# Kernel optimization log

Hardware: AMD Instinct MI355X
Metric: run time of the kernel (lower is better)

Reference implementation:

```python
import jax, jax.numpy as jnp
import numpy as np

B_, S_, D_ = 2, 1024, 1024
EXPAND = 2
D_INNER = EXPAND * D_            # 2048
HEADDIM = 64
NHEADS = D_INNER // HEADDIM      # 32
D_STATE = 64
NGROUPS = 1
D_CONV = 4
CONV_DIM = D_INNER + 2 * NGROUPS * D_STATE      # 2176
D_IN_PROJ = 2 * D_INNER + 2 * NGROUPS * D_STATE + NHEADS  # 4256
H_MLP = 8 * D_                   # GatedMLP fc_1 out (scale * d_model)


def setup_inputs() -> dict:
    key = jax.random.key(0)
    ks = jax.random.split(key, 12)
    n = lambda k, shp, s=0.02: jax.random.normal(k, shp, dtype=jnp.float32) * s
    return {
        "x": jax.random.normal(ks[0], (B_, S_, D_), dtype=jnp.float32),
        "in_proj_w": n(ks[1], (D_IN_PROJ, D_)),
        "conv_w": n(ks[2], (CONV_DIM, D_CONV), 0.2),
        "conv_b": jnp.zeros((CONV_DIM,), jnp.float32),
        "dt_bias": jax.random.normal(ks[3], (NHEADS,), dtype=jnp.float32) * 0.5 - 2.0,
        "A_log": jnp.log(1.0 + 15.0 * jax.random.uniform(ks[4], (NHEADS,), dtype=jnp.float32)),
        "D": jax.random.normal(ks[5], (NHEADS,), dtype=jnp.float32) * 0.1 + 1.0,
        "ssm_norm_w": jnp.ones((D_INNER,), jnp.float32),
        "out_proj_w": n(ks[6], (D_, D_INNER)),
        "rms_w": jnp.ones((D_,), jnp.float32),
        "fc1_w": n(ks[7], (H_MLP, D_)),
        "fc2_w": n(ks[8], (D_, H_MLP // 2)),
    }


def _rms(x, w, eps=1e-5):
    return x * jax.lax.rsqrt(jnp.mean(x * x, axis=-1, keepdims=True) + eps) * w


def _mamba(x, in_proj_w, conv_w, conv_b, dt_bias, A_log, D, ssm_norm_w, out_proj_w):
    b, s, _ = x.shape
    zxbcdt = x @ in_proj_w.T                         # [b,s,D_IN_PROJ]
    z = zxbcdt[..., :D_INNER]
    xBC = zxbcdt[..., D_INNER:D_INNER + CONV_DIM]
    dt_raw = zxbcdt[..., -NHEADS:]
    # causal depthwise conv1d + SiLU
    xc = jnp.pad(jnp.transpose(xBC, (0, 2, 1)), ((0, 0), (0, 0), (D_CONV - 1, 0)))
    xc = jax.lax.conv_general_dilated(xc, conv_w[:, None, :], (1,), 'VALID',
                                      feature_group_count=CONV_DIM,
                                      dimension_numbers=('NCH', 'OIH', 'NCH'))
    xBC = jax.nn.silu(jnp.transpose(xc, (0, 2, 1)) + conv_b)
    xs = xBC[..., :D_INNER].reshape(b, s, NHEADS, HEADDIM)
    Bm = xBC[..., D_INNER:D_INNER + D_STATE]         # [b,s,n] (ngroups=1)
    Cm = xBC[..., D_INNER + D_STATE:]
    dt = jax.nn.softplus(dt_raw + dt_bias)           # [b,s,h]
    dA = jnp.exp(dt * (-jnp.exp(A_log)))             # [b,s,h]
    dtx = dt[..., None] * xs                          # [b,s,h,p]

    def step(h, inp):
        dA_t, dtx_t, B_t, C_t = inp
        h = h * dA_t[:, :, None, None] + jnp.einsum('bhp,bn->bhpn', dtx_t, B_t)
        y = jnp.einsum('bhpn,bn->bhp', h, C_t)
        return h, y

    h0 = jnp.zeros((b, NHEADS, HEADDIM, D_STATE), x.dtype)
    _, y = jax.lax.scan(step, h0, (jnp.transpose(dA, (1, 0, 2)),
                                   jnp.transpose(dtx, (1, 0, 2, 3)),
                                   jnp.transpose(Bm, (1, 0, 2)),
                                   jnp.transpose(Cm, (1, 0, 2))))
    y = jnp.transpose(y, (1, 0, 2, 3)) + D[None, None, :, None] * xs
    y = y.reshape(b, s, D_INNER) * jax.nn.silu(z)    # gated
    y = _rms(y, ssm_norm_w)
    return y @ out_proj_w.T


def reference(x, in_proj_w, conv_w, conv_b, dt_bias, A_log, D, ssm_norm_w,
              out_proj_w, rms_w, fc1_w, fc2_w):
    # x = x + mamba(x)
    x = x + _mamba(x, in_proj_w, conv_w, conv_b, dt_bias, A_log, D, ssm_norm_w, out_proj_w)
    # x = x + GatedMLP(RMSNorm(x))
    xn = _rms(x, rms_w)
    h1 = xn @ fc1_w.T
    a, g = jnp.split(h1, 2, axis=-1)
    m = (a * jax.nn.silu(g)) @ fc2_w.T
    return x + m
```

## Files before the change

kernel.cpp:

```cpp
#include <hip/hip_runtime.h>
#include <math.h>

typedef unsigned short u16;
typedef __attribute__((ext_vector_type(8))) __bf16 bf16x8;
typedef __attribute__((ext_vector_type(4))) float f32x4;
typedef __attribute__((ext_vector_type(4))) u16 u16x4;
typedef __attribute__((ext_vector_type(8))) u16 u16x8;
typedef __attribute__((ext_vector_type(4))) float float4v;

constexpr int kS = 1024;
constexpr int kD = 1024;
constexpr int kDinner = 2048;
constexpr int kHeads = 32;
constexpr int kConvDim = 2176;
constexpr int kDproj = 4256;
constexpr int kDprojPad = 4352;
constexpr int kRows = 2048;
constexpr int kHmlp = 8192;
constexpr int kHhalf = 4096;
constexpr int kL = 64;
constexpr int kNC = 16;

__device__ __forceinline__ float bf2f(u16 u) {
    return __builtin_bit_cast(float, (unsigned int)u << 16);
}
__device__ __forceinline__ u16 f2bf(float f) {
    unsigned int u = __builtin_bit_cast(unsigned int, f);
    u += 0x7fffu + ((u >> 16) & 1u);
    return (u16)(u >> 16);
}
__device__ __forceinline__ float silu_(float x) { return x / (1.f + __expf(-x)); }

__device__ __forceinline__ void gld16(const u16* g, u16* l) {
    __builtin_amdgcn_global_load_lds(
        (const __attribute__((address_space(1))) void*)g,
        (__attribute__((address_space(3))) void*)l, 16, 0, 0);
}

constexpr int kB1 = kRows * kD / 4;
constexpr int kB2 = kB1 + kDprojPad * kD / 4;
constexpr int kB3 = kB2 + kD * kDinner / 4;
constexpr int kB4 = kB3 + kHmlp * kD / 4;
constexpr int kB5 = kB4 + kD * kHhalf / 4;
__global__ __launch_bounds__(256)
void cast_all_kernel(const float* __restrict__ x, const float* __restrict__ w1,
                     const float* __restrict__ w2, const float* __restrict__ w3,
                     const float* __restrict__ w4, u16* __restrict__ xbf,
                     u16* __restrict__ w1bf, u16* __restrict__ w2bf,
                     u16* __restrict__ w3bf, u16* __restrict__ w4bf) {
    int i = blockIdx.x * 256 + threadIdx.x;
    const float* src;
    u16* dst;
    int j;
    if (i < kB1) {
        j = i; src = x; dst = xbf;
    } else if (i < kB2) {
        j = i - kB1;
        int e = j * 4, row = e >> 10, col = e & 1023;
        u16x4 o = {0, 0, 0, 0};
        if (row < kDproj) {
            float4v v = *(const float4v*)(w1 + (size_t)row * kD + col);
            o.x = f2bf(v.x); o.y = f2bf(v.y); o.z = f2bf(v.z); o.w = f2bf(v.w);
        }
        ((u16x4*)w1bf)[j] = o;
        return;
    } else if (i < kB3) {
        j = i - kB2; src = w2; dst = w2bf;
    } else if (i < kB4) {
        j = i - kB3;
        int e = j * 4, row = e >> 10, col4 = (e & 1023) >> 2;
        int p = (row < kHhalf) ? row : row - kHhalf;
        int permrow = (p >> 4) * 32 + (p & 15) + ((row < kHhalf) ? 0 : 16);
        float4v v = ((const float4v*)w3)[j];
        u16x4 o;
        o.x = f2bf(v.x); o.y = f2bf(v.y); o.z = f2bf(v.z); o.w = f2bf(v.w);
        ((u16x4*)w3bf)[permrow * 256 + col4] = o;
        return;
    } else {
        j = i - kB4; src = w4; dst = w4bf;
    }
    float4v v = ((const float4v*)src)[j];
    u16x4 o;
    o.x = f2bf(v.x); o.y = f2bf(v.y); o.z = f2bf(v.z); o.w = f2bf(v.w);
    ((u16x4*)dst)[j] = o;
}

template <bool OUT_BF16, bool GATED = false>
__global__ __launch_bounds__(256)
void gemm_bt(const u16* __restrict__ A, const u16* __restrict__ W,
             void* __restrict__ Cout, const float* __restrict__ resid,
             int M, int N, int K) {
    __shared__ u16 As[2][128 * 32];
    __shared__ u16 Bs[2][128 * 32];
    const int tid = threadIdx.x;
    const int lane = tid & 63;
    const int w = __builtin_amdgcn_readfirstlane(tid >> 6);
    const int wm = w >> 1, wn = w & 1;
    const int bm = blockIdx.y * 128;
    const int bn = blockIdx.x * 128;
    const int z = blockIdx.z;
    const int Kchunk = K / gridDim.z;
    const int k0 = z * Kchunk;

    f32x4 acc[4][4];
#pragma unroll
    for (int i = 0; i < 4; i++)
#pragma unroll
        for (int j = 0; j < 4; j++) acc[i][j] = {0.f, 0.f, 0.f, 0.f};

    const int srow = lane >> 2;
    const int scol = (lane & 3) * 8;
    const u16* gA = A + (size_t)(bm + w * 32 + srow) * K + k0 + scol;
    const u16* gB = W + (size_t)(bn + w * 32 + srow) * K + k0 + scol;
    const size_t rstep = (size_t)16 * K;

    const int sbase0 = (w * 32) * 32;
    const int sbase1 = (w * 32 + 16) * 32;
    const int fra = (lane & 15) * 32 + (lane >> 4) * 8;

    gld16(gA, &As[0][sbase0]);
    gld16(gA + rstep, &As[0][sbase1]);
    gld16(gB, &Bs[0][sbase0]);
    gld16(gB + rstep, &Bs[0][sbase1]);

    const int nk = Kchunk >> 5;
    for (int i = 0; i < nk; i++) {
        const int cur = i & 1, nxt = cur ^ 1;
        __syncthreads();
        if (i + 1 < nk) {
            int kt2 = (i + 1) * 32;
            gld16(gA + kt2, &As[nxt][sbase0]);
            gld16(gA + kt2 + rstep, &As[nxt][sbase1]);
            gld16(gB + kt2, &Bs[nxt][sbase0]);
            gld16(gB + kt2 + rstep, &Bs[nxt][sbase1]);
        }
        bf16x8 av[4], bv[4];
#pragma unroll
        for (int mi = 0; mi < 4; mi++)
            av[mi] = *(const bf16x8*)&As[cur][(wm * 64 + mi * 16) * 32 + fra];
#pragma unroll
        for (int ni = 0; ni < 4; ni++)
            bv[ni] = *(const bf16x8*)&Bs[cur][(wn * 64 + ni * 16) * 32 + fra];
#pragma unroll
        for (int mi = 0; mi < 4; mi++)
#pragma unroll
            for (int ni = 0; ni < 4; ni++)
                acc[mi][ni] = __builtin_amdgcn_mfma_f32_16x16x32_bf16(av[mi], bv[ni], acc[mi][ni], 0, 0, 0);
    }

    const int rb = bm + wm * 64 + ((lane >> 4) << 2);
    const int cb = bn + wn * 64 + (lane & 15);
    if (GATED) {
        u16* Cb = (u16*)Cout;
        const int NG = N >> 1;
        const int gc0 = ((bn + wn * 64) >> 1) + (lane & 15);
#pragma unroll
        for (int mi = 0; mi < 4; mi++) {
#pragma unroll
            for (int p = 0; p < 2; p++) {
#pragma unroll
                for (int r = 0; r < 4; r++) {
                    float a = acc[mi][2 * p][r];
                    float g = acc[mi][2 * p + 1][r];
                    Cb[(size_t)(rb + mi * 16 + r) * NG + gc0 + p * 16] =
                        f2bf(a * silu_(g));
                }
            }
        }
        return;
    }
    float* Cf = (float*)Cout + (size_t)z * M * N;
    u16* Cb = (u16*)Cout;
#pragma unroll
    for (int mi = 0; mi < 4; mi++) {
#pragma unroll
        for (int ni = 0; ni < 4; ni++) {
#pragma unroll
            for (int r = 0; r < 4; r++) {
                size_t offo = (size_t)(rb + mi * 16 + r) * N + (cb + ni * 16);
                float v = acc[mi][ni][r];
                if (resid) v += resid[offo];
                if (OUT_BF16) Cb[offo] = f2bf(v);
                else Cf[offo] = v;
            }
        }
    }
}

__global__ __launch_bounds__(256)
void splitk_reduce_kernel(const float* __restrict__ Cp, const float* __restrict__ resid,
                          float* __restrict__ out, int mn4) {
    int i = blockIdx.x * 256 + threadIdx.x;
    if (i >= mn4) return;
    constexpr size_t MN = (size_t)kRows * kD;
    float4v s0 = ((const float4v*)Cp)[i];
    float4v s1 = ((const float4v*)(Cp + MN))[i];
    float4v s2 = ((const float4v*)(Cp + 2 * MN))[i];
    float4v s3 = ((const float4v*)(Cp + 3 * MN))[i];
    float4v r = ((const float4v*)resid)[i];
    float4v o;
    o.x = s0.x + s1.x + s2.x + s3.x + r.x;
    o.y = s0.y + s1.y + s2.y + s3.y + r.y;
    o.z = s0.z + s1.z + s2.z + s3.z + r.z;
    o.w = s0.w + s1.w + s2.w + s3.w + r.w;
    ((float4v*)out)[i] = o;
}

__global__ __launch_bounds__(256)
void reduce_rms_kernel(const float* __restrict__ Cp, const float* __restrict__ resid,
                       float* __restrict__ x2, const float* __restrict__ rmsw,
                       u16* __restrict__ xnbf) {
    const int row = blockIdx.x;
    const int tid = threadIdx.x;
    constexpr size_t MN = (size_t)kRows * kD;
    size_t i = (size_t)row * (kD / 4) + tid;
    float4v s0 = ((const float4v*)Cp)[i];
    float4v s1 = ((const float4v*)(Cp + MN))[i];
    float4v s2 = ((const float4v*)(Cp + 2 * MN))[i];
    float4v s3 = ((const float4v*)(Cp + 3 * MN))[i];
    float4v r = ((const float4v*)resid)[i];
    float4v v;
    v.x = s0.x + s1.x + s2.x + s3.x + r.x;
    v.y = s0.y + s1.y + s2.y + s3.y + r.y;
    v.z = s0.z + s1.z + s2.z + s3.z + r.z;
    v.w = s0.w + s1.w + s2.w + s3.w + r.w;
    ((float4v*)x2)[i] = v;
    float ss = v.x * v.x + v.y * v.y + v.z * v.z + v.w * v.w;
#pragma unroll
    for (int off = 32; off > 0; off >>= 1) ss += __shfl_down(ss, off);
    __shared__ float red[4];
    int wv = tid >> 6, lane = tid & 63;
    if (lane == 0) red[wv] = ss;
    __syncthreads();
    ss = red[0] + red[1] + red[2] + red[3];
    float rstd = rsqrtf(ss * (1.f / kD) + 1e-5f);
    float4v wv4 = ((const float4v*)rmsw)[tid];
    u16x4 o;
    o.x = f2bf(v.x * rstd * wv4.x);
    o.y = f2bf(v.y * rstd * wv4.y);
    o.z = f2bf(v.z * rstd * wv4.z);
    o.w = f2bf(v.w * rstd * wv4.w);
    ((u16x4*)xnbf)[i] = o;
}

__global__ __launch_bounds__(256)
void convdt_kernel(const u16* __restrict__ zxbf, const float* __restrict__ convw,
                   const float* __restrict__ convb, u16* __restrict__ xsbf,
                   float* __restrict__ BCf, const float* __restrict__ dt_bias,
                   const float* __restrict__ A_log, float* __restrict__ dtf,
                   float* __restrict__ dAf) {
    int c = blockIdx.x * 256 + threadIdx.x;
    int row = blockIdx.y;
    if (c >= kConvDim + kHeads) return;
    if (c < kConvDim) {
        int s = row & (kS - 1);
        float acc = convb[c];
#pragma unroll
        for (int j = 0; j < 4; j++) {
            int sj = s - 3 + j;
            if (sj >= 0)
                acc += bf2f(zxbf[(size_t)(row - 3 + j) * kDprojPad + kDinner + c]) * convw[c * 4 + j];
        }
        float v = silu_(acc);
        if (c < kDinner) xsbf[(size_t)row * kDinner + c] = f2bf(v);
        else BCf[(size_t)row * 128 + (c - kDinner)] = v;
    } else {
        int h = c - kConvDim;
        float raw = bf2f(zxbf[(size_t)row * kDprojPad + (kDinner + kConvDim) + h]) + dt_bias[h];
        float dt = (raw > 20.f) ? raw : log1pf(__expf(raw));
        float dA = __expf(-dt * __expf(A_log[h]));
        dtf[(size_t)row * kHeads + h] = dt;
        dAf[(size_t)row * kHeads + h] = dA;
    }
}

__global__ __launch_bounds__(256)
void scan_chunk_kernel(const u16* __restrict__ xsbf, const float* __restrict__ BCf,
                       const float* __restrict__ dtf, const float* __restrict__ dAf,
                       const float* __restrict__ Dv, u16* __restrict__ ysbf,
                       float* __restrict__ Pf, float* __restrict__ Scf) {
    const int c = blockIdx.x, h = blockIdx.y, b = blockIdx.z;
    const int tid = threadIdx.x;
    const int lane = tid & 63;
    const int nq = tid >> 6;
    const int p = nq * 16 + (lane & 15);
    const int ng = lane >> 4;

    __shared__ float BC_lds[kL * 136];
    __shared__ u16 xs_lds[kL * 64];
    __shared__ float dA_lds[kL];
    __shared__ float dt_lds[kL];
    __shared__ u16 ybuf[kL * 64];

    const int row0 = b * kS + c * kL;

#pragma unroll
    for (int i = 0; i < 8; i++) {
        int e4 = i * 256 + tid;
        int t = e4 >> 5;
        int col = (e4 & 31) * 4;
        float4v v = *(const float4v*)(BCf + (size_t)(row0 + t) * 128 + col);
        int dst = t * 136 + (col < 64 ? col : col + 4);
        *(float4v*)&BC_lds[dst] = v;
    }
#pragma unroll
    for (int i = 0; i < 2; i++) {
        int e8 = i * 256 + tid;
        int t = e8 >> 3, col8 = (e8 & 7) * 8;
        *(u16x8*)&xs_lds[t * 64 + col8] =
            *(const u16x8*)(xsbf + (size_t)(row0 + t) * kDinner + h * 64 + col8);
    }
    if (tid < kL) {
        dt_lds[tid] = dtf[(size_t)(row0 + tid) * kHeads + h];
        dA_lds[tid] = dAf[(size_t)(row0 + tid) * kHeads + h];
    }
    __syncthreads();

    float hst[16];
#pragma unroll
    for (int j = 0; j < 16; j++) hst[j] = 0.f;
    float P = 1.f;
    const float Dh = Dv[h];

    for (int t = 0; t < kL; t++) {
        float dAv = dA_lds[t];
        float dtv = dt_lds[t];
        float xsv = bf2f(xs_lds[t * 64 + p]);
        float dtx = dtv * xsv;
        P *= dAv;
        const float* Bt = &BC_lds[t * 136 + ng * 16];
        const float* Ct = Bt + 68;
        float yp = 0.f;
#pragma unroll
        for (int j = 0; j < 16; j++) {
            float Bn = Bt[j];
            float Cn = Ct[j];
            hst[j] = hst[j] * dAv + dtx * Bn;
            yp += hst[j] * Cn;
        }
        yp += __shfl_xor(yp, 16);
        yp += __shfl_xor(yp, 32);
        if (ng == 0) ybuf[t * 64 + p] = f2bf(yp + Dh * xsv);
        if (tid == 0) Pf[(size_t)(row0 + t) * kHeads + h] = P;
    }
    __syncthreads();

#pragma unroll
    for (int i = 0; i < 2; i++) {
        int e8 = i * 256 + tid;
        int t = e8 >> 3, col8 = (e8 & 7) * 8;
        *(u16x8*)(ysbf + (size_t)(row0 + t) * kDinner + h * 64 + col8) =
            *(u16x8*)&ybuf[t * 64 + col8];
    }
    const int bhc = (b * 32 + h) * kNC + c;
    float* Sdst = Scf + (size_t)bhc * 4096 + p * 64 + ng * 16;
#pragma unroll
    for (int j = 0; j < 16; j += 4) {
        f32x4 v = {hst[j], hst[j + 1], hst[j + 2], hst[j + 3]};
        *(f32x4*)(Sdst + j) = v;
    }
}

__global__ __launch_bounds__(256)
void chunk_state_kernel(const float* __restrict__ Scf, const float* __restrict__ Pf,
                        float* __restrict__ Hinf) {
    const int bh = blockIdx.x;
    const int b = bh >> 5, h = bh & 31;
    const int tid = threadIdx.x;
    float hreg[16];
#pragma unroll
    for (int k = 0; k < 16; k++) hreg[k] = 0.f;
    for (int c = 0; c < kNC - 1; c++) {
        float Q = Pf[(size_t)(b * kS + c * kL + kL - 1) * kHeads + h];
        size_t sbase = (size_t)(bh * kNC + c) * 4096;
        size_t dbase = (size_t)(bh * kNC + c + 1) * 4096;
#pragma unroll
        for (int k = 0; k < 16; k++) {
            float s = Scf[sbase + k * 256 + tid];
            hreg[k] = Q * hreg[k] + s;
            Hinf[dbase + k * 256 + tid] = hreg[k];
        }
    }
}

__global__ __launch_bounds__(256)
void chunk_corr_kernel(const float* __restrict__ Hinf, const float* __restrict__ BCf,
                       const float* __restrict__ Pf, u16* __restrict__ ysbf) {
    const int c = blockIdx.x + 1;
    const int h = blockIdx.y, b = blockIdx.z;
    const int tid = threadIdx.x;
    const int lane = tid & 63, wq = tid >> 6;
    __shared__ float Hin_lds[64 * 65];
    __shared__ float C_lds[kL * 64];
    const int bh = b * 32 + h;
    const size_t hbase = (size_t)(bh * kNC + c) * 4096;
#pragma unroll
    for (int k = 0; k < 16; k++) {
        int e = k * 256 + tid;
        Hin_lds[(e >> 6) * 65 + (e & 63)] = Hinf[hbase + e];
    }
    const int row0 = b * kS + c * kL;
#pragma unroll
    for (int k = 0; k < 4; k++) {
        int e4 = k * 256 + tid;
        int t = e4 >> 4, n4 = (e4 & 15) * 4;
        *(float4v*)&C_lds[t * 64 + n4] =
            *(const float4v*)(BCf + (size_t)(row0 + t) * 128 + 64 + n4);
    }
    __syncthreads();

    float hr[64];
#pragma unroll
    for (int n = 0; n < 64; n++) hr[n] = Hin_lds[lane * 65 + n];

    for (int tt = 0; tt < 16; tt++) {
        int t = wq * 16 + tt;
        float corr = 0.f;
#pragma unroll
        for (int n4 = 0; n4 < 16; n4++) {
            float4v cv = *(const float4v*)&C_lds[t * 64 + n4 * 4];
            corr += cv.x * hr[n4 * 4] + cv.y * hr[n4 * 4 + 1] +
                    cv.z * hr[n4 * 4 + 2] + cv.w * hr[n4 * 4 + 3];
        }
        float Pt = Pf[(size_t)(row0 + t) * kHeads + h];
        size_t yoff = (size_t)(row0 + t) * kDinner + h * 64 + lane;
        ysbf[yoff] = f2bf(bf2f(ysbf[yoff]) + Pt * corr);
    }
}

__global__ __launch_bounds__(256)
void gatenorm_kernel(const u16* __restrict__ ysbf, const u16* __restrict__ zxbf,
                     const float* __restrict__ normw, u16* __restrict__ ybf) {
    const int row = blockIdx.x;
    const int tid = threadIdx.x;
    float v[8];
    float ss = 0.f;
#pragma unroll
    for (int i = 0; i < 8; i++) {
        int idx = i * 256 + tid;
        float y = bf2f(ysbf[(size_t)row * kDinner + idx]);
        float z = bf2f(zxbf[(size_t)row * kDprojPad + idx]);
        v[i] = y * silu_(z);
        ss += v[i] * v[i];
    }
#pragma unroll
    for (int off = 32; off > 0; off >>= 1) ss += __shfl_down(ss, off);
    __shared__ float red[4];
    int wv = tid >> 6, lane = tid & 63;
    if (lane == 0) red[wv] = ss;
    __syncthreads();
    ss = red[0] + red[1] + red[2] + red[3];
    float rstd = rsqrtf(ss * (1.f / kDinner) + 1e-5f);
#pragma unroll
    for (int i = 0; i < 8; i++) {
        int idx = i * 256 + tid;
        ybf[(size_t)row * kDinner + idx] = f2bf(v[i] * rstd * normw[idx]);
    }
}

extern "C" void kernel_launch(void* const* d_in, const int* in_sizes, int n_in,
                              void* d_out, int out_size, void* d_ws, size_t ws_size,
                              hipStream_t stream) {
    const float* x         = (const float*)d_in[0];
    const float* in_proj_w = (const float*)d_in[1];
    const float* conv_w    = (const float*)d_in[2];
    const float* conv_b    = (const float*)d_in[3];
    const float* dt_bias   = (const float*)d_in[4];
    const float* A_log     = (const float*)d_in[5];
    const float* Dvec      = (const float*)d_in[6];
    const float* ssm_norm_w= (const float*)d_in[7];
    const float* out_proj_w= (const float*)d_in[8];
    const float* rms_w     = (const float*)d_in[9];
    const float* fc1_w     = (const float*)d_in[10];
    const float* fc2_w     = (const float*)d_in[11];
    float* out = (float*)d_out;

    char* ws = (char*)d_ws;
    size_t off = 0;
    auto alloc = [&](size_t bytes) -> void* {
        void* p = ws + off;
        off += (bytes + 255) & ~(size_t)255;
        return p;
    };
    u16*   xbf  = (u16*)alloc((size_t)kRows * kD * 2);
    u16*   w1bf = (u16*)alloc((size_t)kDprojPad * kD * 2);
    u16*   w2bf = (u16*)alloc((size_t)kD * kDinner * 2);
    u16*   w3bf = (u16*)alloc((size_t)kHmlp * kD * 2);
    u16*   w4bf = (u16*)alloc((size_t)kD * kHhalf * 2);
    u16*   zxbf = (u16*)alloc((size_t)kRows * kDprojPad * 2);
    u16*   xsbf = (u16*)alloc((size_t)kRows * kDinner * 2);
    float* BCf  = (float*)alloc((size_t)kRows * 128 * 4);
    float* dtf  = (float*)alloc((size_t)kRows * kHeads * 4);
    float* dAf  = (float*)alloc((size_t)kRows * kHeads * 4);
    float* Pf   = (float*)alloc((size_t)kRows * kHeads * 4);
    u16*   ysbf = (u16*)alloc((size_t)kRows * kDinner * 2);
    u16*   ybf  = (u16*)alloc((size_t)kRows * kDinner * 2);
    float* x2   = (float*)alloc((size_t)kRows * kD * 4);
    u16*   xnbf = (u16*)alloc((size_t)kRows * kD * 2);
    u16*   h1bf = (u16*)alloc((size_t)kRows * kHmlp * 2);
    u16*   gbf  = (u16*)alloc((size_t)kRows * kHhalf * 2);
    float* Scf  = (float*)gbf;
    float* Hinf = (float*)h1bf;
    float* Cp   = (float*)h1bf;
    (void)ws_size; (void)in_sizes; (void)n_in; (void)out_size;

    cast_all_kernel<<<kB5 / 256, 256, 0, stream>>>(
        x, in_proj_w, out_proj_w, fc1_w, fc2_w, xbf, w1bf, w2bf, w3bf, w4bf);

    gemm_bt<true><<<dim3(kDprojPad / 128, kRows / 128, 1), 256, 0, stream>>>(
        xbf, w1bf, zxbf, nullptr, kRows, kDprojPad, kD);

    convdt_kernel<<<dim3((kConvDim + kHeads + 255) / 256, kRows), 256, 0, stream>>>(
        zxbf, conv_w, conv_b, xsbf, BCf, dt_bias, A_log, dtf, dAf);

    scan_chunk_kernel<<<dim3(kNC, kHeads, 2), 256, 0, stream>>>(
        xsbf, BCf, dtf, dAf, Dvec, ysbf, Pf, Scf);
    chunk_state_kernel<<<64, 256, 0, stream>>>(Scf, Pf, Hinf);
    chunk_corr_kernel<<<dim3(kNC - 1, kHeads, 2), 256, 0, stream>>>(Hinf, BCf, Pf, ysbf);

    gatenorm_kernel<<<kRows, 256, 0, stream>>>(ysbf, zxbf, ssm_norm_w, ybf);

    gemm_bt<false><<<dim3(kD / 128, kRows / 128, 4), 256, 0, stream>>>(
        ybf, w2bf, Cp, nullptr, kRows, kD, kDinner);
    reduce_rms_kernel<<<kRows, 256, 0, stream>>>(Cp, x, x2, rms_w, xnbf);

    gemm_bt<true, true><<<dim3(kHmlp / 128, kRows / 128, 1), 256, 0, stream>>>(
        xnbf, w3bf, gbf, nullptr, kRows, kHmlp, kD);

    gemm_bt<false><<<dim3(kD / 128, kRows / 128, 4), 256, 0, stream>>>(
        gbf, w4bf, Cp, nullptr, kRows, kD, kHhalf);
    splitk_reduce_kernel<<<(kRows * kD / 4 + 255) / 256, 256, 0, stream>>>(
        Cp, x2, out, kRows * kD / 4);
}
```

Before: 378.7 us.

## Add 256x256 pipelined MFMA kernel for gated fc1 GEMM

Replaces the 128x128 gated fc1 GEMM with a new 512-thread kernel computing 256x256 tiles. It double-buffers LDS with async global-to-LDS loads interleaved into four phases per K-tile, uses explicit vmcnt waits and barriers with raised priority around the MFMA bursts, and applies a swizzled block-to-tile mapping. The silu gating is fused into the epilogue. The aim is more data reuse per load and better overlap of memory with compute. In exchange it needs more registers and LDS per block and relies on a hand-tuned wait-count schedule that is fragile to get right.

```diff
diff --git a/kernel.cpp b/kernel.cpp
--- a/kernel.cpp
+++ b/kernel.cpp
@@ -182,6 +182,136 @@
                 if (resid) v += resid[offo];
                 if (OUT_BF16) Cb[offo] = f2bf(v);
                 else Cf[offo] = v;
+            }
+        }
+    }
+}
+
+#define VMCNT6 asm volatile("s_waitcnt vmcnt(6)" ::: "memory")
+#define VMCNT0 asm volatile("s_waitcnt vmcnt(0)" ::: "memory")
+
+__global__ __launch_bounds__(512, 2)
+void gemm256_gated(const u16* __restrict__ A, const u16* __restrict__ W,
+                   u16* __restrict__ Cout, int M, int N, int K) {
+    __shared__ u16 lds[2][2][2][2][4096];
+    const int tid = threadIdx.x;
+    const int lane = tid & 63;
+    const int w = __builtin_amdgcn_readfirstlane(tid >> 6);
+    const int wm = w >> 2;
+    const int wn = w & 3;
+    const int wnh = wn >> 1, wnl = wn & 1;
+
+    const int ntn = N >> 8;
+    const int ntiles = (M >> 8) * ntn;
+    const int qchunk = ntiles >> 3;
+    const int lin = blockIdx.x;
+    const int swz = (lin & 7) * qchunk + (lin >> 3);
+    const int bm = (swz / ntn) << 8;
+    const int bn = (swz % ntn) << 8;
+
+    const int rst = tid >> 2, sst = tid & 3;
+    const int vst = (((rst >> 1) & 1) << 1) | ((rst >> 2) & 1);
+    const u16* gA0 = A + (size_t)(bm + rst) * K + ((sst ^ vst) << 3);
+    const u16* gB0 = W + (size_t)(bn + rst) * K + ((sst ^ vst) << 3);
+    const size_t hstep = (size_t)128 * K;
+    const int wq512 = w * 512;
+
+    const int r0a = lane & 15, slot = lane >> 4;
+    const int v2a = (((r0a >> 1) & 1) << 1) | ((r0a >> 2) & 1);
+    const int fro = r0a * 32 + ((slot ^ v2a) << 3);
+
+    f32x4 acc[8][4];
+#pragma unroll
+    for (int i = 0; i < 8; i++)
+#pragma unroll
+        for (int j = 0; j < 4; j++) acc[i][j] = {0.f, 0.f, 0.f, 0.f};
+    bf16x8 bv[4];
+    const int nt = K >> 6;
+
+#define STAGE(d, mat, kh, kt)                                               \
+    { const u16* g_ = ((mat) ? gB0 : gA0) + (size_t)(kt) * 64 + (kh) * 32;  \
+      gld16(g_, &lds[d][mat][0][kh][wq512]);                                \
+      gld16(g_ + hstep, &lds[d][mat][1][kh][wq512]); }
+
+#define LDA_FRAG(dst, d, kh, mfb)                                           \
+    _Pragma("unroll") for (int i_ = 0; i_ < 4; i_++)                        \
+        dst[i_] = *(const bf16x8*)&lds[d][0][wm][kh][((mfb) + i_) * 512 + fro];
+
+#define LDB_FRAG(d, kh)                                                     \
+    _Pragma("unroll") for (int i_ = 0; i_ < 4; i_++)                        \
+        bv[i_] = *(const bf16x8*)&lds[d][1][wnh][kh][wnl * 2048 + i_ * 512 + fro];
+
+#define PHASE_TAIL(g4)                                                      \
+    __builtin_amdgcn_sched_barrier(0);                                      \
+    __builtin_amdgcn_s_barrier();                                           \
+    __builtin_amdgcn_sched_barrier(0);                                      \
+    __builtin_amdgcn_s_setprio(1);                                          \
+    _Pragma("unroll") for (int i_ = 0; i_ < 4; i_++)                        \
+        _Pragma("unroll") for (int n_ = 0; n_ < 4; n_++)                    \
+            acc[(g4) * 4 + i_][n_] = __builtin_amdgcn_mfma_f32_16x16x32_bf16( \
+                av[i_], bv[n_], acc[(g4) * 4 + i_][n_], 0, 0, 0);           \
+    __builtin_amdgcn_s_setprio(0);                                          \
+    __builtin_amdgcn_sched_barrier(0);                                      \
+    __builtin_amdgcn_s_barrier();                                           \
+    __builtin_amdgcn_sched_barrier(0);
+
+#define TILE(T, D)                                                          \
+    {                                             \
+      { bf16x8 av[4]; LDB_FRAG(D, 0); LDA_FRAG(av, D, 0, 0);                \
+        if ((T) + 1 < nt) STAGE(D ^ 1, 0, 1, (T) + 1);                      \
+        PHASE_TAIL(0) }                                                     \
+                                                  \
+      { bf16x8 av[4]; LDA_FRAG(av, D, 0, 4);                                \
+        if ((T) + 2 < nt) STAGE(D, 1, 0, (T) + 2);                          \
+        PHASE_TAIL(1) }                                                     \
+                                                  \
+      { bf16x8 av[4]; LDB_FRAG(D, 1); LDA_FRAG(av, D, 1, 0);                \
+        if ((T) + 2 < nt) STAGE(D, 0, 0, (T) + 2);                          \
+        PHASE_TAIL(0) }                                                     \
+                                  \
+      { bf16x8 av[4]; LDA_FRAG(av, D, 1, 4);                                \
+        if ((T) + 2 < nt) STAGE(D, 1, 1, (T) + 2);                          \
+        if ((T) + 2 < nt) { VMCNT6; } else if ((T) + 1 < nt) { VMCNT0; }    \
+        PHASE_TAIL(1) }                                                     \
+    }
+
+    STAGE(0, 1, 0, 0);
+    STAGE(0, 0, 0, 0);
+    STAGE(0, 1, 1, 0);
+    STAGE(0, 0, 1, 0);
+    STAGE(1, 1, 0, 1);
+    STAGE(1, 0, 0, 1);
+    STAGE(1, 1, 1, 1);
+    VMCNT6;
+    __builtin_amdgcn_sched_barrier(0);
+    __builtin_amdgcn_s_barrier();
+    __builtin_amdgcn_sched_barrier(0);
+
+    for (int tt = 0; tt < nt; tt += 2) {
+        TILE(tt, 0)
+        TILE(tt + 1, 1)
+    }
+
+#undef TILE
+#undef PHASE_TAIL
+#undef LDB_FRAG
+#undef LDA_FRAG
+#undef STAGE
+
+    u16* Cb = Cout;
+    const int NG = N >> 1;
+    const int rb = bm + wm * 128 + ((lane >> 4) << 2);
+    const int gc0 = ((bn + wn * 64) >> 1) + (lane & 15);
+#pragma unroll
+    for (int mf = 0; mf < 8; mf++) {
+#pragma unroll
+        for (int p = 0; p < 2; p++) {
+#pragma unroll
+            for (int r = 0; r < 4; r++) {
+                float a = acc[mf][2 * p][r];
+                float g = acc[mf][2 * p + 1][r];
+                Cb[(size_t)(rb + mf * 16 + r) * NG + gc0 + p * 16] =
+                    f2bf(a * silu_(g));
             }
         }
     }
@@ -524,8 +654,8 @@
         ybf, w2bf, Cp, nullptr, kRows, kD, kDinner);
     reduce_rms_kernel<<<kRows, 256, 0, stream>>>(Cp, x, x2, rms_w, xnbf);
 
-    gemm_bt<true, true><<<dim3(kHmlp / 128, kRows / 128, 1), 256, 0, stream>>>(
-        xnbf, w3bf, gbf, nullptr, kRows, kHmlp, kD);
+    gemm256_gated<<<dim3((kRows >> 8) * (kHmlp >> 8)), 512, 0, stream>>>(
+        xnbf, w3bf, gbf, kRows, kHmlp, kD);
 
     gemm_bt<false><<<dim3(kD / 128, kRows / 128, 4), 256, 0, stream>>>(
         gbf, w4bf, Cp, nullptr, kRows, kD, kHhalf);
```

Result: no change. 372.0 us (-1.8%).
